# Performance work log

Hardware: AMD Instinct MI355X
Metric: run time of the kernel (lower is better)

The kernel has to match this reference:

```python
import jax, jax.numpy as jnp
import numpy as np

START_TAG = 7
STOP_TAG = 8
NEG = -10000.0  # matches torch.full((1,K), -10000.) in the original


def setup_inputs() -> dict:
    key = jax.random.key(0)
    k1, k2, k3, k4 = jax.random.split(key, 4)
    B, T, K = 1024, 2048, 9  # K = output_dim + 2 (START/STOP hardcoded as 7/8)
    feats = jax.random.normal(k1, (B, T, K), dtype=jnp.float32)
    tags = jax.random.randint(k2, (B, T), 0, 7)            # valid labels 0..6
    lengths = jax.random.randint(k3, (B,), 1, T + 1)        # per-sentence lengths >= 1
    transitions = jax.random.normal(k4, (K, K), dtype=jnp.float32)
    transitions = transitions.at[START_TAG, :].set(NEG)     # never transition into START
    transitions = transitions.at[:, STOP_TAG].set(NEG)      # never transition out of STOP
    return {"feats": feats, "transitions": transitions, "tags": tags, "lengths": lengths}


def _crf_nll(feats, transitions, tags, lengths):
    # feats: [B,T,K] emissions, transitions[j,i] = score of i -> j
    B, T, K = feats.shape

    def fwd_one(feat, length):
        # CRF forward algorithm (log partition), vectorized over tags,
        # lax.scan over time; masked past `length` to emulate feats[:x_len].
        alpha0 = jnp.full((K,), NEG, feat.dtype).at[START_TAG].set(0.0)

        def step(alpha, inp):
            t, f = inp
            # alpha_new[j] = logsumexp_i(alpha[i] + transitions[j,i]) + feat[t,j]
            new = jax.nn.logsumexp(alpha[None, :] + transitions, axis=1) + f
            return jnp.where(t < length, new, alpha), None

        alpha, _ = jax.lax.scan(step, alpha0, (jnp.arange(T), feat))
        return jax.nn.logsumexp(alpha + transitions[STOP_TAG])

    fwd_scores = jax.vmap(fwd_one)(feats, lengths)  # [B]

    def gold_one(feat, tg, length):
        # _score_sentence: sum_t trans[tags[t], tags[t-1]] + feat[t, tags[t]]
        prev = jnp.concatenate([jnp.array([START_TAG], tg.dtype), tg[:-1]])
        step_scores = transitions[tg, prev] + jnp.take_along_axis(feat, tg[:, None], axis=1)[:, 0]
        mask = jnp.arange(tg.shape[0]) < length
        last = tg[length - 1]
        return jnp.sum(jnp.where(mask, step_scores, 0.0)) + transitions[STOP_TAG, last]

    gold_scores = jax.vmap(gold_one)(feats, tags, lengths)  # [B]

    # neg_log_likelihood accumulates (forward - gold) per sentence, then / n
    return jnp.mean(fwd_scores - gold_scores)


def reference(feats, transitions, tags, lengths):
    return _crf_nll(feats, transitions, tags, lengths)
```

## Files before the change

### kernel.cpp

```cpp
#include <hip/hip_runtime.h>


#define START_TAG 7
#define STOP_TAG  8
#define KDIM      9
#define NS        7
#define CHUNKS    32
#define NEGINF    (-1e30f)

__device__ __forceinline__ float rfl(float x) {
    return __int_as_float(__builtin_amdgcn_readfirstlane(__float_as_int(x)));
}

__global__ __launch_bounds__(256) void crf_fused_kernel(
    const float* __restrict__ feats,
    const float* __restrict__ trans,
    const int*   __restrict__ tags,
    const int*   __restrict__ lengths,
    float* __restrict__ out,
    int B, int T)
{
    __shared__ float s_trans[81];
    __shared__ float s_E[49];
    __shared__ float s_M[CHUNKS * 64];
    __shared__ float s_gold[4];

    const int tid = threadIdx.x;
    const int b   = blockIdx.x;

    if (tid < 81) s_trans[tid] = trans[tid];
    if (tid >= 128 && tid < 177) {
        int k = tid - 128;
        s_E[k] = __expf(trans[(k / 7) * 9 + (k % 7)]);
    }
    __syncthreads();

    const int    len   = lengths[b];
    const int*   tg    = tags  + (size_t)b * T;
    const float* fbase = feats + (size_t)b * T * KDIM;
    const int    Lb    = (len > 1) ? ((len - 1 + CHUNKS - 1) / CHUNKS) : 1;

    {
        int per = (T >> 8) > 0 ? (T >> 8) : 1;
        int t0  = tid * per;
        float g = 0.f;
        if (t0 < len) {
            int te   = min(t0 + per, len);
            int prev = (t0 == 0) ? START_TAG : tg[t0 - 1];
            if (per == 8) {
                #pragma unroll
                for (int k = 0; k < 8; ++k) {
                    int t   = t0 + k;
                    int tc  = min(t, te - 1);
                    int cur = tg[tc];
                    float v = s_trans[cur * 9 + prev] + fbase[(size_t)tc * KDIM + cur];
                    g += (t < te) ? v : 0.f;
                    prev = cur;
                }
            } else {
                for (int k = 0; k < per; ++k) {
                    int t   = t0 + k;
                    int tc  = min(t, te - 1);
                    int cur = tg[tc];
                    float v = s_trans[cur * 9 + prev] + fbase[(size_t)tc * KDIM + cur];
                    g += (t < te) ? v : 0.f;
                    prev = cur;
                }
            }
            if (len - 1 >= t0 && len - 1 < t0 + per)
                g += s_trans[STOP_TAG * 9 + tg[len - 1]];
        }
        #pragma unroll
        for (int off = 32; off > 0; off >>= 1) g += __shfl_xor(g, off, 64);
        if ((tid & 63) == 0) s_gold[tid >> 6] = g;
    }

    {
        const int lane8  = tid & 7;
        const int c      = tid >> 3;
        const int tstart = 1 + c * Lb;
        const int tend   = min(tstart + Lb, len);

        if (lane8 < NS) {
            float* Mw = s_M + c * 64;
            if (tstart < tend) {
                float E[49];
                #pragma unroll
                for (int k = 0; k < 49; ++k) E[k] = rfl(s_E[k]);

                int baddr[NS];
                #pragma unroll
                for (int j = 0; j < NS; ++j) baddr[j] = (((tid & 56) | j) << 2);

                float p[NS];
                #pragma unroll
                for (int j = 0; j < NS; ++j) p[j] = (j == lane8) ? 1.f : 0.f;
                float s = 0.f;
                int rem = tend - tstart;

                const float* fp = fbase + (size_t)tstart * KDIM + lane8;

                #define CRF_MAT(EF) do {                                        \
                    float q[NS];                                                \
                    _Pragma("unroll")                                           \
                    for (int j = 0; j < NS; ++j) {                              \
                        float acc = E[j * 7] * p[0];                            \
                        _Pragma("unroll")                                       \
                        for (int i = 1; i < NS; ++i)                            \
                            acc = fmaf(E[j * 7 + i], p[i], acc);                \
                        q[j] = acc;                                             \
                    }                                                           \
                    _Pragma("unroll")                                           \
                    for (int j = 0; j < NS; ++j) p[j] = q[j] * EF[j];           \
                } while (0)

                #define CRF_BCAST(DST, XF) do {                                 \
                    float _e = __expf(XF);                                      \
                    _Pragma("unroll")                                           \
                    for (int j = 0; j < NS; ++j)                                \
                        DST[j] = __int_as_float(                                \
                            __builtin_amdgcn_ds_bpermute(                       \
                                baddr[j], __float_as_int(_e)));                 \
                } while (0)

                #define CRF_STEP(XF) do {                                       \
                    float _ef[NS];                                              \
                    CRF_BCAST(_ef, XF);                                         \
                    CRF_MAT(_ef);                                               \
                } while (0)

                #define CRF_RENORM() do {                                       \
                    float m = p[0];                                             \
                    _Pragma("unroll")                                           \
                    for (int j = 1; j < NS; ++j) m = fmaxf(m, p[j]);            \
                    float rm = __builtin_amdgcn_rcpf(m);                        \
                    _Pragma("unroll")                                           \
                    for (int j = 0; j < NS; ++j) p[j] *= rm;                    \
                    s += __logf(m);                                             \
                } while (0)

                int o1 = KDIM * min(1, rem - 1);
                int o2 = KDIM * min(2, rem - 1);
                int o3 = KDIM * min(3, rem - 1);
                float x0 = fp[0], x1 = fp[o1], x2 = fp[o2], x3 = fp[o3];
                fp += 4 * KDIM;

                while (rem >= 8) {
                    float y0 = fp[0], y1 = fp[KDIM], y2 = fp[2 * KDIM], y3 = fp[3 * KDIM];
                    fp += 4 * KDIM;
                    float efA[NS], efB[NS], efC[NS], efD[NS];
                    CRF_BCAST(efA, x0);
                    CRF_BCAST(efB, x1);
                    CRF_BCAST(efC, x2);
                    CRF_BCAST(efD, x3);
                    CRF_MAT(efA); CRF_MAT(efB); CRF_MAT(efC); CRF_MAT(efD);
                    CRF_RENORM();
                    x0 = y0; x1 = y1; x2 = y2; x3 = y3;
                    rem -= 4;
                }
                if (rem > 4) {
                    int e1 = KDIM * min(1, rem - 5);
                    int e2 = KDIM * min(2, rem - 5);
                    float y0 = fp[0], y1 = fp[e1], y2 = fp[e2];
                    float efA[NS], efB[NS], efC[NS], efD[NS];
                    CRF_BCAST(efA, x0);
                    CRF_BCAST(efB, x1);
                    CRF_BCAST(efC, x2);
                    CRF_BCAST(efD, x3);
                    CRF_MAT(efA); CRF_MAT(efB); CRF_MAT(efC); CRF_MAT(efD);
                    CRF_RENORM();
                    x0 = y0; x1 = y1; x2 = y2;
                    rem -= 4;
                }
                CRF_STEP(x0);
                if (rem > 1) CRF_STEP(x1);
                if (rem > 2) CRF_STEP(x2);
                if (rem > 3) CRF_STEP(x3);

                #pragma unroll
                for (int j = 0; j < NS; ++j)
                    Mw[j * 8 + lane8] = __logf(p[j]) + s;

                #undef CRF_MAT
                #undef CRF_BCAST
                #undef CRF_STEP
                #undef CRF_RENORM
            } else {
                #pragma unroll
                for (int j = 0; j < NS; ++j)
                    Mw[j * 8 + lane8] = (j == lane8) ? 0.f : NEGINF;
            }
        }
    }
    __syncthreads();

    if (tid < 8) {
        const int  lane  = tid;
        const bool isrow = (lane < NS);
        const int  row   = isrow ? lane : 0;

        float a[NS];
        #pragma unroll
        for (int i = 0; i < NS; ++i)
            a[i] = s_trans[i * 9 + START_TAG] + fbase[i];
        float S;
        {
            float mm = fmaxf(fmaxf(fmaxf(a[0], a[1]), fmaxf(a[2], a[3])),
                             fmaxf(fmaxf(a[4], a[5]), a[6]));
            S = mm;
            #pragma unroll
            for (int i = 0; i < NS; ++i) a[i] -= mm;
        }

        int nc = (len > 1) ? ((len - 1 + Lb - 1) / Lb) : 0;
        if (nc > CHUNKS) nc = CHUNKS;

        const float* Mr0 = s_M + row * 8;
        float4 mA = *(const float4*)(Mr0);
        float4 mB = *(const float4*)(Mr0 + 4);
        for (int cc = 0; cc < nc; ++cc) {
            int cn = min(cc + 1, CHUNKS - 1);
            float4 nA = *(const float4*)(Mr0 + cn * 64);
            float4 nB = *(const float4*)(Mr0 + cn * 64 + 4);
            float t0 = mA.x + a[0], t1 = mA.y + a[1], t2 = mA.z + a[2];
            float t3 = mA.w + a[3], t4 = mB.x + a[4], t5 = mB.y + a[5];
            float t6 = mB.z + a[6];
            float tm = fmaxf(fmaxf(fmaxf(t0, t1), fmaxf(t2, t3)),
                             fmaxf(fmaxf(t4, t5), t6));
            float e0 = __expf(t0 - tm), e1 = __expf(t1 - tm), e2 = __expf(t2 - tm);
            float e3 = __expf(t3 - tm), e4 = __expf(t4 - tm), e5 = __expf(t5 - tm);
            float e6 = __expf(t6 - tm);
            float sum = ((e0 + e1) + (e2 + e3)) + ((e4 + e5) + e6);
            float na = tm + __logf(sum);
            float b0 = __shfl(na, 0, 8), b1 = __shfl(na, 1, 8), b2 = __shfl(na, 2, 8);
            float b3 = __shfl(na, 3, 8), b4 = __shfl(na, 4, 8), b5 = __shfl(na, 5, 8);
            float b6 = __shfl(na, 6, 8);
            float mm = fmaxf(fmaxf(fmaxf(b0, b1), fmaxf(b2, b3)),
                             fmaxf(fmaxf(b4, b5), b6));
            a[0] = b0 - mm; a[1] = b1 - mm; a[2] = b2 - mm;
            a[3] = b3 - mm; a[4] = b4 - mm; a[5] = b5 - mm;
            a[6] = b6 - mm;
            S += mm;
            mA = nA; mB = nB;
        }

        if (lane == 0) {
            float t0 = a[0] + s_trans[STOP_TAG * 9 + 0];
            float t1 = a[1] + s_trans[STOP_TAG * 9 + 1];
            float t2 = a[2] + s_trans[STOP_TAG * 9 + 2];
            float t3 = a[3] + s_trans[STOP_TAG * 9 + 3];
            float t4 = a[4] + s_trans[STOP_TAG * 9 + 4];
            float t5 = a[5] + s_trans[STOP_TAG * 9 + 5];
            float t6 = a[6] + s_trans[STOP_TAG * 9 + 6];
            float tm = fmaxf(fmaxf(fmaxf(t0, t1), fmaxf(t2, t3)),
                             fmaxf(fmaxf(t4, t5), t6));
            float sum = ((__expf(t0 - tm) + __expf(t1 - tm)) +
                         (__expf(t2 - tm) + __expf(t3 - tm))) +
                        ((__expf(t4 - tm) + __expf(t5 - tm)) + __expf(t6 - tm));
            float fwd = S + tm + __logf(sum);
            float g = s_gold[0] + s_gold[1] + s_gold[2] + s_gold[3];
            atomicAdd(out, (fwd - g) * (1.0f / (float)B));
        }
    }
}

__global__ void init_out_kernel(float* out) {
    if (threadIdx.x == 0) out[0] = 0.f;
}

extern "C" void kernel_launch(void* const* d_in, const int* in_sizes, int n_in,
                              void* d_out, int out_size, void* d_ws, size_t ws_size,
                              hipStream_t stream) {
    const float* feats   = (const float*)d_in[0];
    const float* trans   = (const float*)d_in[1];
    const int*   tags    = (const int*)d_in[2];
    const int*   lengths = (const int*)d_in[3];

    int B = in_sizes[3];
    int T = in_sizes[2] / B;

    init_out_kernel<<<1, 64, 0, stream>>>((float*)d_out);
    crf_fused_kernel<<<B, 256, 0, stream>>>(
        feats, trans, tags, lengths, (float*)d_out, B, T);
}
```

Baseline: 154.5 us.

## Double chunk count to 64 with 512 threads and tree-combine chunk matrices

Raises the number of time chunks per sentence from 32 to 64 and the block size from 256 to 512 threads, so each chunk's serial scan is shorter. Adds a parallel per-wave combine stage in which each wave folds its 8 chunk transfer matrices together using ds_bpermute log-semiring products. The final serial combine then walks 8 wave results instead of up to 32 chunks. Gold scoring is spread across 512 threads with 4 steps each. This buys more parallelism at the cost of extra matrix-combine work, a larger LDS footprint and higher register pressure from the launch bounds.

```diff
diff --git a/kernel.cpp b/kernel.cpp
--- a/kernel.cpp
+++ b/kernel.cpp
@@ -5,14 +5,14 @@
 #define STOP_TAG  8
 #define KDIM      9
 #define NS        7
-#define CHUNKS    32
+#define CHUNKS    64
 #define NEGINF    (-1e30f)
 
 __device__ __forceinline__ float rfl(float x) {
     return __int_as_float(__builtin_amdgcn_readfirstlane(__float_as_int(x)));
 }
 
-__global__ __launch_bounds__(256) void crf_fused_kernel(
+__global__ __launch_bounds__(512, 4) void crf_fused_kernel(
     const float* __restrict__ feats,
     const float* __restrict__ trans,
     const int*   __restrict__ tags,
@@ -23,7 +23,7 @@
     __shared__ float s_trans[81];
     __shared__ float s_E[49];
     __shared__ float s_M[CHUNKS * 64];
-    __shared__ float s_gold[4];
+    __shared__ float s_gold[8];
 
     const int tid = threadIdx.x;
     const int b   = blockIdx.x;
@@ -41,15 +41,15 @@
     const int    Lb    = (len > 1) ? ((len - 1 + CHUNKS - 1) / CHUNKS) : 1;
 
     {
-        int per = (T >> 8) > 0 ? (T >> 8) : 1;
+        int per = T >> 9; if (per < 1) per = 1;
         int t0  = tid * per;
         float g = 0.f;
         if (t0 < len) {
             int te   = min(t0 + per, len);
             int prev = (t0 == 0) ? START_TAG : tg[t0 - 1];
-            if (per == 8) {
-                #pragma unroll
-                for (int k = 0; k < 8; ++k) {
+            if (per == 4) {
+                #pragma unroll
+                for (int k = 0; k < 4; ++k) {
                     int t   = t0 + k;
                     int tc  = min(t, te - 1);
                     int cur = tg[tc];
@@ -194,6 +194,41 @@
     }
     __syncthreads();
 
+    {
+        const int l = tid & 63;
+        const int w = tid >> 6;
+        const int i = l & 7;
+        float* seg = s_M + w * 512;
+
+        float A = seg[l];
+        int baddr[NS];
+        #pragma unroll
+        for (int k = 0; k < NS; ++k) baddr[k] = ((k << 3) | i) << 2;
+
+        #pragma unroll
+        for (int c = 1; c < 8; ++c) {
+            const float* Mr = seg + c * 64 + (l & 56);
+            float4 r0 = *(const float4*)(Mr);
+            float4 r1 = *(const float4*)(Mr + 4);
+            float ac[NS];
+            #pragma unroll
+            for (int k = 0; k < NS; ++k)
+                ac[k] = __int_as_float(__builtin_amdgcn_ds_bpermute(
+                            baddr[k], __float_as_int(A)));
+            float t0 = r0.x + ac[0], t1 = r0.y + ac[1], t2 = r0.z + ac[2];
+            float t3 = r0.w + ac[3], t4 = r1.x + ac[4], t5 = r1.y + ac[5];
+            float t6 = r1.z + ac[6];
+            float tm = fmaxf(fmaxf(fmaxf(t0, t1), fmaxf(t2, t3)),
+                             fmaxf(fmaxf(t4, t5), t6));
+            float sum = ((__expf(t0 - tm) + __expf(t1 - tm)) +
+                         (__expf(t2 - tm) + __expf(t3 - tm))) +
+                        ((__expf(t4 - tm) + __expf(t5 - tm)) + __expf(t6 - tm));
+            A = tm + __logf(sum);
+        }
+        seg[l] = A;
+    }
+    __syncthreads();
+
     if (tid < 8) {
         const int  lane  = tid;
         const bool isrow = (lane < NS);
@@ -212,16 +247,14 @@
             for (int i = 0; i < NS; ++i) a[i] -= mm;
         }
 
-        int nc = (len > 1) ? ((len - 1 + Lb - 1) / Lb) : 0;
-        if (nc > CHUNKS) nc = CHUNKS;
-
         const float* Mr0 = s_M + row * 8;
         float4 mA = *(const float4*)(Mr0);
         float4 mB = *(const float4*)(Mr0 + 4);
-        for (int cc = 0; cc < nc; ++cc) {
-            int cn = min(cc + 1, CHUNKS - 1);
-            float4 nA = *(const float4*)(Mr0 + cn * 64);
-            float4 nB = *(const float4*)(Mr0 + cn * 64 + 4);
+        #pragma unroll
+        for (int w = 0; w < 8; ++w) {
+            int wn = min(w + 1, 7);
+            float4 nA = *(const float4*)(Mr0 + wn * 512);
+            float4 nB = *(const float4*)(Mr0 + wn * 512 + 4);
             float t0 = mA.x + a[0], t1 = mA.y + a[1], t2 = mA.z + a[2];
             float t3 = mA.w + a[3], t4 = mB.x + a[4], t5 = mB.y + a[5];
             float t6 = mB.z + a[6];
@@ -231,7 +264,7 @@
             float e3 = __expf(t3 - tm), e4 = __expf(t4 - tm), e5 = __expf(t5 - tm);
             float e6 = __expf(t6 - tm);
             float sum = ((e0 + e1) + (e2 + e3)) + ((e4 + e5) + e6);
-            float na = tm + __logf(sum);
+            float na = isrow ? (tm + __logf(sum)) : NEGINF;
             float b0 = __shfl(na, 0, 8), b1 = __shfl(na, 1, 8), b2 = __shfl(na, 2, 8);
             float b3 = __shfl(na, 3, 8), b4 = __shfl(na, 4, 8), b5 = __shfl(na, 5, 8);
             float b6 = __shfl(na, 6, 8);
@@ -258,7 +291,8 @@
                          (__expf(t2 - tm) + __expf(t3 - tm))) +
                         ((__expf(t4 - tm) + __expf(t5 - tm)) + __expf(t6 - tm));
             float fwd = S + tm + __logf(sum);
-            float g = s_gold[0] + s_gold[1] + s_gold[2] + s_gold[3];
+            float g = (s_gold[0] + s_gold[1] + s_gold[2] + s_gold[3]) +
+                      (s_gold[4] + s_gold[5] + s_gold[6] + s_gold[7]);
             atomicAdd(out, (fwd - g) * (1.0f / (float)B));
         }
     }
@@ -280,6 +314,6 @@
     int T = in_sizes[2] / B;
 
     init_out_kernel<<<1, 64, 0, stream>>>((float*)d_out);
-    crf_fused_kernel<<<B, 256, 0, stream>>>(
+    crf_fused_kernel<<<B, 512, 0, stream>>>(
         feats, trans, tags, lengths, (float*)d_out, B, T);
 }
```

Result: faster. 142.4 us (-7.9%).
